# Kernel tuning notes

Measured on AMD Instinct MI355X. Metric: run time of the kernel, lower is better.

Reference implementation:

```python
import jax, jax.numpy as jnp
import numpy as np
import math

B, C_IN, N_SEL, N_DROP, HEADS = 4, 128, 1024, 1024, 4
Q_OUT = K_OUT = V_OUT = 256
N = N_SEL + N_DROP


def setup_inputs() -> dict:
    key = jax.random.key(0)
    ks = jax.random.split(key, 8)
    pcd_up = jax.random.normal(ks[0], (B, C_IN, N), jnp.float32)
    points_select = jax.random.normal(ks[1], (B, C_IN, N_SEL), jnp.float32)
    points_drop = jax.random.normal(ks[2], (B, C_IN, N_DROP), jnp.float32)
    # per-batch permutation of [0, N) split into select/drop halves (collision-free scatter)
    perms = jax.vmap(lambda k: jax.random.permutation(k, N))(jax.random.split(ks[3], B))
    idx_select = perms[:, None, :N_SEL].astype(jnp.int32)
    idx_drop = perms[:, None, N_SEL:].astype(jnp.int32)
    scale = 1.0 / math.sqrt(C_IN)
    Wq = jax.random.normal(ks[4], (Q_OUT, C_IN), jnp.float32) * scale
    Wk = jax.random.normal(ks[5], (K_OUT, C_IN), jnp.float32) * scale
    Wv = jax.random.normal(ks[6], (V_OUT, C_IN), jnp.float32) * scale
    Wskip = jax.random.normal(ks[7], (V_OUT, C_IN), jnp.float32) * scale
    return {"pcd_up": pcd_up, "points_select": points_select, "points_drop": points_drop,
            "idx_select": idx_select, "idx_drop": idx_drop,
            "Wq": Wq, "Wk": Wk, "Wv": Wv, "Wskip": Wskip}


def _concat_by_idx(a, b, idx_a, idx_b):
    # scatter columns of concat([a,b]) to positions given by concat([idx_a, idx_b])
    src = jnp.concatenate([a, b], axis=-1)            # (B, C, N)
    idx = jnp.concatenate([idx_a, idx_b], axis=-1)[:, 0, :]  # (B, N)
    return jax.vmap(lambda s, i: jnp.zeros_like(s).at[:, i].set(s))(src, idx)


def reference(pcd_up, points_select, points_drop, idx_select, idx_drop, Wq, Wk, Wv, Wskip):
    b, _, n = pcd_up.shape
    x = _concat_by_idx(points_select, points_drop, idx_select, idx_drop)  # (B, C_in, N)
    # 1x1 convs (no bias) == channel matmuls, then split heads: (B, H, D, N)
    q = jnp.einsum('oc,bcn->bon', Wq, x).reshape(b, HEADS, Q_OUT // HEADS, n)
    k = jnp.einsum('oc,bcn->bon', Wk, x).reshape(b, HEADS, K_OUT // HEADS, n)
    v = jnp.einsum('oc,bcn->bon', Wv, x).reshape(b, HEADS, V_OUT // HEADS, n)
    energy = jnp.einsum('bhdn,bhdm->bhnm', q, k)      # (B, H, N, N)
    attn = jax.nn.softmax(energy / math.sqrt(Q_OUT // HEADS), axis=-1)
    out = jnp.einsum('bhnm,bhdm->bhnd', attn, v)      # (B, H, N, Dv)
    out = out.transpose(0, 2, 1, 3).reshape(b, n, V_OUT).transpose(0, 2, 1)  # (B, V_out, N)
    skip = jnp.einsum('oc,bcn->bon', Wskip, pcd_up)   # (B, V_out, N)
    return skip + out
```

## Files before the change

### kernel.cpp

```cpp
#include <hip/hip_runtime.h>
#include <hip/hip_bf16.h>
#include <math.h>

#define B_    4
#define C_IN_ 128
#define N_    2048
#define NSEL_ 1024
#define H_    4
#define KS_   2

typedef __bf16 bf16;
typedef __bf16 bf16x2 __attribute__((ext_vector_type(2)));
typedef __bf16 bf16x4 __attribute__((ext_vector_type(4)));
typedef __bf16 bf16x8 __attribute__((ext_vector_type(8)));
typedef float  f32x4  __attribute__((ext_vector_type(4)));

__global__ __launch_bounds__(256) void prep_kernel(
    const int* __restrict__ isel, const int* __restrict__ idrp,
    const float* __restrict__ Wq, const float* __restrict__ Wk,
    const float* __restrict__ Wv, const float* __restrict__ Ws,
    int* __restrict__ inv, bf16* __restrict__ Wbf)
{
    const int blk = blockIdx.x;
    if (blk < 128) {
        int e = blk * 256 + threadIdx.x;
        int which = e >> 13, idx = e & 8191;
        const float* Wx = (which == 0) ? Wq : (which == 1) ? Wk
                        : (which == 2) ? Wv : Ws;
        float4 v = *(const float4*)(Wx + (size_t)idx * 4);
        bf16x4 o; o[0] = (bf16)v.x; o[1] = (bf16)v.y; o[2] = (bf16)v.z; o[3] = (bf16)v.w;
        *(bf16x4*)(Wbf + (size_t)which * 32768 + (size_t)idx * 4) = o;
    } else {
        int g = (blk - 128) * 256 + threadIdx.x;
        int b = g >> 11, j = g & (N_ - 1);
        int pos = (j < NSEL_) ? isel[b * NSEL_ + j] : idrp[b * NSEL_ + (j - NSEL_)];
        inv[b * N_ + (pos & (N_ - 1))] = j;
    }
}

#define XSTR 136

__global__ __launch_bounds__(256) void qkv_mfma_kernel(
    const float* __restrict__ pcd, const float* __restrict__ sel,
    const float* __restrict__ drop, const bf16* __restrict__ Wbf,
    bf16* __restrict__ qT, bf16* __restrict__ kTt, bf16* __restrict__ vTt)
{
    const int ntile = blockIdx.x;
    const int which = blockIdx.y >> 1;
    const int rh    = blockIdx.y & 1;
    const int b     = blockIdx.z;
    const int tid   = threadIdx.x;
    const int w     = tid >> 6;
    const int lane  = tid & 63;
    const int quad  = lane >> 4;
    const int lc    = lane & 15;
    const int n0    = ntile * 64;

    __shared__ __align__(16) bf16 xT[64 * XSTR];

    const float* srcp; int rstride;
    if (ntile < 16) { srcp = sel  + (size_t)b * C_IN_ * NSEL_ + n0;           rstride = NSEL_; }
    else            { srcp = drop + (size_t)b * C_IN_ * NSEL_ + (n0 - NSEL_); rstride = NSEL_; }

    #pragma unroll
    for (int k = 0; k < 4; ++k) {
        int e  = tid + k * 256;
        int cp = e >> 4, nq = e & 15;
        int c0 = cp * 2;
        float4 v0 = *(const float4*)(srcp + (size_t)c0 * rstride + nq * 4);
        float4 v1 = *(const float4*)(srcp + (size_t)(c0 + 1) * rstride + nq * 4);
        int cc = c0 ^ ((nq & 3) << 3);
        float a0[4] = {v0.x, v0.y, v0.z, v0.w};
        float a1[4] = {v1.x, v1.y, v1.z, v1.w};
        #pragma unroll
        for (int i = 0; i < 4; ++i) {
            int n = nq * 4 + i;
            bf16x2 t; t[0] = (bf16)a0[i]; t[1] = (bf16)a1[i];
            *(bf16x2*)&xT[n * XSTR + cc] = t;
        }
    }
    __syncthreads();

    const bf16* wbase = Wbf + (size_t)which * 256 * 128;
    const int rbase = rh * 128 + w * 32;

    f32x4 acc[8];
    #pragma unroll
    for (int i = 0; i < 8; ++i) acc[i] = (f32x4){0.f, 0.f, 0.f, 0.f};

    #pragma unroll
    for (int kq = 0; kq < 4; ++kq) {
        bf16x8 wf[2], xA[4];
        #pragma unroll
        for (int ot = 0; ot < 2; ++ot)
            wf[ot] = *(const bf16x8*)(wbase + (size_t)(rbase + ot * 16 + lc) * 128 + kq * 32 + quad * 8);
        #pragma unroll
        for (int nt = 0; nt < 4; ++nt) {
            int row = nt * 16 + lc;
            int col = (kq * 32 + quad * 8) ^ (((row >> 2) & 3) << 3);
            xA[nt] = *(const bf16x8*)&xT[row * XSTR + col];
        }
        if (which <= 1) {
            #pragma unroll
            for (int nt = 0; nt < 4; ++nt)
                #pragma unroll
                for (int ot = 0; ot < 2; ++ot)
                    acc[nt * 2 + ot] = __builtin_amdgcn_mfma_f32_16x16x32_bf16(xA[nt], wf[ot], acc[nt * 2 + ot], 0, 0, 0);
        } else {
            #pragma unroll
            for (int ot = 0; ot < 2; ++ot)
                #pragma unroll
                for (int nt = 0; nt < 4; ++nt)
                    acc[ot * 4 + nt] = __builtin_amdgcn_mfma_f32_16x16x32_bf16(wf[ot], xA[nt], acc[ot * 4 + nt], 0, 0, 0);
        }
    }

    if (which <= 1) {
        #pragma unroll
        for (int nt = 0; nt < 4; ++nt) {
            #pragma unroll
            for (int ot = 0; ot < 2; ++ot) {
                #pragma unroll
                for (int r = 0; r < 4; ++r) {
                    int n    = n0 + nt * 16 + quad * 4 + r;
                    int rloc = nt * 16 + quad * 4 + r;
                    int o256 = rbase + ot * 16 + lc;
                    int h = o256 >> 6, d = o256 & 63;
                    float val = acc[nt * 2 + ot][r];
                    if (which == 0)
                        qT[((size_t)(b * H_ + h) * N_ + n) * 64 + d] = (bf16)(val * 0.125f);
                    else
                        kTt[(((size_t)(b * H_ + h) * 32 + ntile) << 12) | (rloc << 6) | d] = (bf16)val;
                }
            }
        }
    } else {
        #pragma unroll
        for (int ot = 0; ot < 2; ++ot) {
            #pragma unroll
            for (int r = 0; r < 4; ++r) {
                int o256 = rbase + ot * 16 + quad * 4 + r;
                int h = o256 >> 6, dv = o256 & 63;
                bf16x4 pk;
                #pragma unroll
                for (int nt = 0; nt < 4; ++nt) pk[nt] = (bf16)acc[ot * 4 + nt][r];
                *(bf16x4*)(vTt + ((((size_t)(b * H_ + h) * 32 + ntile) << 12) | (dv << 6) | (lc * 4))) = pk;
            }
        }
    }
}

#define PSTR 72
#define KVSTR 72

__global__ __launch_bounds__(256, 2) void attn_kernel(
    const bf16* __restrict__ qT, const bf16* __restrict__ kTt,
    const bf16* __restrict__ vTt, bf16* __restrict__ Opart,
    float* __restrict__ S_ws)
{
    const int id    = blockIdx.x;
    const int bh    = (id & 7) + 8 * ((id >> 3) & 1);
    const int qb    = (id >> 4) & 15;
    const int c     = id >> 8;
    const int b     = bh >> 2;
    const int h     = bh & 3;
    const int tid   = threadIdx.x;
    const int w     = tid >> 6;
    const int lane  = tid & 63;
    const int quad  = lane >> 4;
    const int lc    = lane & 15;
    const int n0    = qb * 128 + w * 32;

    __shared__ __align__(16) bf16 sK[2][64 * KVSTR];
    __shared__ __align__(16) bf16 sV[2][64 * KVSTR];
    __shared__ __align__(16) bf16 p_lds[4 * 16 * PSTR];
    bf16* pw = &p_lds[w * 16 * PSTR];

    bf16x8 aq[2][2];
    #pragma unroll
    for (int t = 0; t < 2; ++t) {
        const bf16* qp = qT + ((size_t)bh * N_ + n0 + t * 16 + lc) * 64 + quad * 8;
        aq[t][0] = *(const bf16x8*)(qp);
        aq[t][1] = *(const bf16x8*)(qp + 32);
    }

    const bf16* kbase = kTt + (((size_t)bh * 32 + c * 16) << 12);
    const bf16* vbase = vTt + (((size_t)bh * 32 + c * 16) << 12);

    const int l0 = (tid >> 3) * KVSTR + (tid & 7) * 8;
    const int l1 = ((tid >> 3) + 32) * KVSTR + (tid & 7) * 8;

    bf16x8 ldK0 = *(const bf16x8*)(kbase + tid * 8);
    bf16x8 ldK1 = *(const bf16x8*)(kbase + 2048 + tid * 8);
    bf16x8 ldV0 = *(const bf16x8*)(vbase + tid * 8);
    bf16x8 ldV1 = *(const bf16x8*)(vbase + 2048 + tid * 8);

    f32x4 accO[2][4];
    #pragma unroll
    for (int t = 0; t < 2; ++t)
        #pragma unroll
        for (int i = 0; i < 4; ++i) accO[t][i] = (f32x4){0.f, 0.f, 0.f, 0.f};
    float psum[2][4] = {{0.f,0.f,0.f,0.f},{0.f,0.f,0.f,0.f}};

    for (int s = 0; s < 16; ++s) {
        const int buf = s & 1;
        *(bf16x8*)&sK[buf][l0] = ldK0;
        *(bf16x8*)&sK[buf][l1] = ldK1;
        *(bf16x8*)&sV[buf][l0] = ldV0;
        *(bf16x8*)&sV[buf][l1] = ldV1;
        __syncthreads();

        if (s < 15) {
            const bf16* kg = kbase + ((size_t)(s + 1) << 12);
            const bf16* vg = vbase + ((size_t)(s + 1) << 12);
            ldK0 = *(const bf16x8*)(kg + tid * 8);
            ldK1 = *(const bf16x8*)(kg + 2048 + tid * 8);
            ldV0 = *(const bf16x8*)(vg + tid * 8);
            ldV1 = *(const bf16x8*)(vg + 2048 + tid * 8);
        }

        bf16x8 kf[4][2], vf[4][2];
        #pragma unroll
        for (int mt = 0; mt < 4; ++mt) {
            const int rb = (mt * 16 + lc) * KVSTR + quad * 8;
            kf[mt][0] = *(const bf16x8*)&sK[buf][rb];
            kf[mt][1] = *(const bf16x8*)&sK[buf][rb + 32];
            vf[mt][0] = *(const bf16x8*)&sV[buf][rb];
            vf[mt][1] = *(const bf16x8*)&sV[buf][rb + 32];
        }

        #pragma unroll
        for (int t = 0; t < 2; ++t) {
            f32x4 accS[4];
            #pragma unroll
            for (int mt = 0; mt < 4; ++mt) {
                f32x4 z = (f32x4){0.f, 0.f, 0.f, 0.f};
                z = __builtin_amdgcn_mfma_f32_16x16x32_bf16(aq[t][0], kf[mt][0], z, 0, 0, 0);
                z = __builtin_amdgcn_mfma_f32_16x16x32_bf16(aq[t][1], kf[mt][1], z, 0, 0, 0);
                accS[mt] = z;
            }
            #pragma unroll
            for (int r = 0; r < 4; ++r) {
                float sum = 0.f;
                #pragma unroll
                for (int mt = 0; mt < 4; ++mt) {
                    float p = __expf(accS[mt][r]);
                    accS[mt][r] = p;
                    sum += p;
                }
                psum[t][r] += sum;
            }
            #pragma unroll
            for (int r = 0; r < 4; ++r) {
                bf16x4 pk;
                #pragma unroll
                for (int mt = 0; mt < 4; ++mt) pk[mt] = (bf16)accS[mt][r];
                *(bf16x4*)&pw[(quad * 4 + r) * PSTR + lc * 4] = pk;
            }
            bf16x8 ap0 = *(const bf16x8*)(&pw[lc * PSTR + quad * 8]);
            bf16x8 ap1 = *(const bf16x8*)(&pw[lc * PSTR + 32 + quad * 8]);
            #pragma unroll
            for (int dvt = 0; dvt < 4; ++dvt) {
                accO[t][dvt] = __builtin_amdgcn_mfma_f32_16x16x32_bf16(ap0, vf[dvt][0], accO[t][dvt], 0, 0, 0);
                accO[t][dvt] = __builtin_amdgcn_mfma_f32_16x16x32_bf16(ap1, vf[dvt][1], accO[t][dvt], 0, 0, 0);
            }
        }
    }

    #pragma unroll
    for (int t = 0; t < 2; ++t) {
        float inv[4];
        #pragma unroll
        for (int r = 0; r < 4; ++r) {
            float s = psum[t][r];
            #pragma unroll
            for (int off = 1; off < 16; off <<= 1)
                s += __shfl_xor(s, off, 64);
            inv[r] = 1.f / s;
            int n = n0 + t * 16 + quad * 4 + r;
            if (lc == 0)
                S_ws[((size_t)(c * B_ + b) * H_ + h) * N_ + n] = s;
        }
        #pragma unroll
        for (int r = 0; r < 4; ++r) {
            int n = n0 + t * 16 + quad * 4 + r;
            #pragma unroll
            for (int dvt = 0; dvt < 4; ++dvt) {
                int o = h * 64 + dvt * 16 + lc;
                Opart[((size_t)(c * B_ + b) * N_ + n) * 256 + o] = (bf16)(accO[t][dvt][r] * inv[r]);
            }
        }
    }
}

__global__ __launch_bounds__(256) void scatter_kernel(
    const bf16* __restrict__ Opart, const float* __restrict__ S_ws,
    const int* __restrict__ inv, const float* __restrict__ pcd,
    const bf16* __restrict__ Wbf, float* __restrict__ out)
{
    const int ptile = blockIdx.x;
    const int og    = blockIdx.y;
    const int b     = blockIdx.z;
    const int tid   = threadIdx.x;
    const int w     = tid >> 6;
    const int lane  = tid & 63;
    const int quad  = lane >> 4;
    const int lc    = lane & 15;
    const int p0    = ptile * 64;

    __shared__ __align__(16) bf16 xT[64 * XSTR];
    __shared__ __align__(16) bf16 lds[64 * 72];
    __shared__ float wls[KS_][64];
    __shared__ int   jrow[64];

    const float* srcp = pcd + (size_t)b * C_IN_ * N_ + p0;
    #pragma unroll
    for (int k = 0; k < 4; ++k) {
        int e  = tid + k * 256;
        int cp = e >> 4, nq = e & 15;
        int c0 = cp * 2;
        float4 v0 = *(const float4*)(srcp + (size_t)c0 * N_ + nq * 4);
        float4 v1 = *(const float4*)(srcp + (size_t)(c0 + 1) * N_ + nq * 4);
        int cc = c0 ^ ((nq & 3) << 3);
        float a0[4] = {v0.x, v0.y, v0.z, v0.w};
        float a1[4] = {v1.x, v1.y, v1.z, v1.w};
        #pragma unroll
        for (int i = 0; i < 4; ++i) {
            int n = nq * 4 + i;
            bf16x2 t; t[0] = (bf16)a0[i]; t[1] = (bf16)a1[i];
            *(bf16x2*)&xT[n * XSTR + cc] = t;
        }
    }
    if (tid < 64) {
        int row = tid;
        int j = inv[b * N_ + p0 + row] & (N_ - 1);
        jrow[row] = j;
        float sv[KS_]; float denom = 0.f;
        #pragma unroll
        for (int c = 0; c < KS_; ++c) {
            sv[c] = S_ws[((size_t)(c * B_ + b) * H_ + og) * N_ + j];
            denom += sv[c];
        }
        float idn = 1.f / denom;
        #pragma unroll
        for (int c = 0; c < KS_; ++c) wls[c][row] = sv[c] * idn;
    }
    __syncthreads();

    const bf16* wbase = Wbf + (size_t)3 * 256 * 128 + (size_t)(og * 64 + w * 16) * 128;
    f32x4 acc[4];
    #pragma unroll
    for (int i = 0; i < 4; ++i) acc[i] = (f32x4){0.f, 0.f, 0.f, 0.f};
    #pragma unroll
    for (int kq = 0; kq < 4; ++kq) {
        bf16x8 A = *(const bf16x8*)(wbase + (size_t)lc * 128 + kq * 32 + quad * 8);
        #pragma unroll
        for (int nt = 0; nt < 4; ++nt) {
            int row = nt * 16 + lc;
            int col = (kq * 32 + quad * 8) ^ (((row >> 2) & 3) << 3);
            bf16x8 Bf = *(const bf16x8*)&xT[row * XSTR + col];
            acc[nt] = __builtin_amdgcn_mfma_f32_16x16x32_bf16(A, Bf, acc[nt], 0, 0, 0);
        }
    }

    #pragma unroll
    for (int k = 0; k < 2; ++k) {
        int e = tid + k * 256;
        int row = e >> 3, seg = e & 7;
        int j = jrow[row];
        float a8[8];
        #pragma unroll
        for (int i = 0; i < 8; ++i) a8[i] = 0.f;
        #pragma unroll
        for (int c = 0; c < KS_; ++c) {
            bf16x8 v = *(const bf16x8*)(Opart + ((size_t)(c * B_ + b) * N_ + j) * 256 + og * 64 + seg * 8);
            float wgt = wls[c][row];
            #pragma unroll
            for (int i = 0; i < 8; ++i) a8[i] += wgt * (float)v[i];
        }
        bf16x8 o8;
        #pragma unroll
        for (int i = 0; i < 8; ++i) o8[i] = (bf16)a8[i];
        *(bf16x8*)&lds[row * 72 + seg * 8] = o8;
    }
    __syncthreads();

    #pragma unroll
    for (int nt = 0; nt < 4; ++nt) {
        #pragma unroll
        for (int r = 0; r < 4; ++r) {
            int o_loc = w * 16 + quad * 4 + r;
            int p     = nt * 16 + lc;
            float attn = (float)lds[p * 72 + o_loc];
            out[((size_t)b * 256 + og * 64 + o_loc) * N_ + p0 + p] = acc[nt][r] + attn;
        }
    }
}

extern "C" void kernel_launch(void* const* d_in, const int* in_sizes, int n_in,
                              void* d_out, int out_size, void* d_ws, size_t ws_size,
                              hipStream_t stream) {
    const float* pcd  = (const float*)d_in[0];
    const float* sel  = (const float*)d_in[1];
    const float* drop = (const float*)d_in[2];
    const int*   isel = (const int*)d_in[3];
    const int*   idrp = (const int*)d_in[4];
    const float* Wq   = (const float*)d_in[5];
    const float* Wk   = (const float*)d_in[6];
    const float* Wv   = (const float*)d_in[7];
    const float* Ws   = (const float*)d_in[8];
    float* out = (float*)d_out;

    const size_t MB = 1024 * 1024;
    char*  ws    = (char*)d_ws;
    bf16*  qT    = (bf16*)(ws);
    bf16*  kTt   = (bf16*)(ws + 4 * MB);
    bf16*  vTt   = (bf16*)(ws + 8 * MB);
    bf16*  Opart = (bf16*)(ws + 12 * MB);
    float* S_ws  = (float*)(ws + 20 * MB);
    bf16*  Wbf   = (bf16*)(ws + 20 * MB + 256 * 1024);
    int*   inv   = (int*)(ws + 20 * MB + 512 * 1024);

    prep_kernel<<<dim3(160), 256, 0, stream>>>(isel, idrp, Wq, Wk, Wv, Ws, inv, Wbf);
    qkv_mfma_kernel<<<dim3(32, 6, B_), 256, 0, stream>>>(pcd, sel, drop, Wbf,
                                                         qT, kTt, vTt);
    attn_kernel<<<dim3(16 * 16 * KS_), 256, 0, stream>>>(qT, kTt, vTt, Opart, S_ws);
    scatter_kernel<<<dim3(32, 4, B_), 256, 0, stream>>>(Opart, S_ws, inv, pcd, Wbf, out);
}
```

Measured before the change: 117.9 us.

## Double attention query tile per block and move inverse-index build into QKV kernel

The attention kernel now gives each wave 64 query rows instead of 32, so each staged K/V tile in LDS serves twice as many queries. The grid halves to 256 blocks and launch bounds drop to one block per CU, which allows more registers per thread. Separately, the inverse-permutation scatter moves out of the prep kernel into an extra y-slice of the QKV kernel, taking that work off the prep kernel's path. The risks are lower occupancy and fewer blocks than the CU count, which may leave compute units idle and weaken latency hiding.

```diff
diff --git a/kernel.cpp b/kernel.cpp
--- a/kernel.cpp
+++ b/kernel.cpp
@@ -16,40 +16,44 @@
 typedef float  f32x4  __attribute__((ext_vector_type(4)));
 
 __global__ __launch_bounds__(256) void prep_kernel(
-    const int* __restrict__ isel, const int* __restrict__ idrp,
     const float* __restrict__ Wq, const float* __restrict__ Wk,
     const float* __restrict__ Wv, const float* __restrict__ Ws,
-    int* __restrict__ inv, bf16* __restrict__ Wbf)
+    bf16* __restrict__ Wbf)
 {
-    const int blk = blockIdx.x;
-    if (blk < 128) {
-        int e = blk * 256 + threadIdx.x;
-        int which = e >> 13, idx = e & 8191;
-        const float* Wx = (which == 0) ? Wq : (which == 1) ? Wk
-                        : (which == 2) ? Wv : Ws;
-        float4 v = *(const float4*)(Wx + (size_t)idx * 4);
-        bf16x4 o; o[0] = (bf16)v.x; o[1] = (bf16)v.y; o[2] = (bf16)v.z; o[3] = (bf16)v.w;
-        *(bf16x4*)(Wbf + (size_t)which * 32768 + (size_t)idx * 4) = o;
-    } else {
-        int g = (blk - 128) * 256 + threadIdx.x;
-        int b = g >> 11, j = g & (N_ - 1);
-        int pos = (j < NSEL_) ? isel[b * NSEL_ + j] : idrp[b * NSEL_ + (j - NSEL_)];
-        inv[b * N_ + (pos & (N_ - 1))] = j;
-    }
+    int e = blockIdx.x * 256 + threadIdx.x;
+    int which = e >> 13, idx = e & 8191;
+    const float* Wx = (which == 0) ? Wq : (which == 1) ? Wk
+                    : (which == 2) ? Wv : Ws;
+    float4 v = *(const float4*)(Wx + (size_t)idx * 4);
+    bf16x4 o; o[0] = (bf16)v.x; o[1] = (bf16)v.y; o[2] = (bf16)v.z; o[3] = (bf16)v.w;
+    *(bf16x4*)(Wbf + (size_t)which * 32768 + (size_t)idx * 4) = o;
 }
 
 #define XSTR 136
 
 __global__ __launch_bounds__(256) void qkv_mfma_kernel(
-    const float* __restrict__ pcd, const float* __restrict__ sel,
-    const float* __restrict__ drop, const bf16* __restrict__ Wbf,
-    bf16* __restrict__ qT, bf16* __restrict__ kTt, bf16* __restrict__ vTt)
+    const float* __restrict__ sel, const float* __restrict__ drop,
+    const bf16* __restrict__ Wbf,
+    const int* __restrict__ isel, const int* __restrict__ idrp,
+    bf16* __restrict__ qT, bf16* __restrict__ kTt, bf16* __restrict__ vTt,
+    int* __restrict__ inv)
 {
     const int ntile = blockIdx.x;
+    const int b     = blockIdx.z;
+    const int tid   = threadIdx.x;
+
+    if (blockIdx.y == 6) {
+        if (ntile < 8) {
+            int j = ntile * 256 + tid;
+            int pos = (j < NSEL_) ? isel[b * NSEL_ + j]
+                                  : idrp[b * NSEL_ + (j - NSEL_)];
+            inv[b * N_ + (pos & (N_ - 1))] = j;
+        }
+        return;
+    }
+
     const int which = blockIdx.y >> 1;
     const int rh    = blockIdx.y & 1;
-    const int b     = blockIdx.z;
-    const int tid   = threadIdx.x;
     const int w     = tid >> 6;
     const int lane  = tid & 63;
     const int quad  = lane >> 4;
@@ -153,15 +157,15 @@
 #define PSTR 72
 #define KVSTR 72
 
-__global__ __launch_bounds__(256, 2) void attn_kernel(
+__global__ __launch_bounds__(256, 1) void attn_kernel(
     const bf16* __restrict__ qT, const bf16* __restrict__ kTt,
     const bf16* __restrict__ vTt, bf16* __restrict__ Opart,
     float* __restrict__ S_ws)
 {
     const int id    = blockIdx.x;
     const int bh    = (id & 7) + 8 * ((id >> 3) & 1);
-    const int qb    = (id >> 4) & 15;
-    const int c     = id >> 8;
+    const int qb    = (id >> 4) & 7;
+    const int c     = id >> 7;
     const int b     = bh >> 2;
     const int h     = bh & 3;
     const int tid   = threadIdx.x;
@@ -169,16 +173,16 @@
     const int lane  = tid & 63;
     const int quad  = lane >> 4;
     const int lc    = lane & 15;
-    const int n0    = qb * 128 + w * 32;
+    const int n0    = qb * 256 + w * 64;
 
     __shared__ __align__(16) bf16 sK[2][64 * KVSTR];
     __shared__ __align__(16) bf16 sV[2][64 * KVSTR];
     __shared__ __align__(16) bf16 p_lds[4 * 16 * PSTR];
     bf16* pw = &p_lds[w * 16 * PSTR];
 
-    bf16x8 aq[2][2];
-    #pragma unroll
-    for (int t = 0; t < 2; ++t) {
+    bf16x8 aq[4][2];
+    #pragma unroll
+    for (int t = 0; t < 4; ++t) {
         const bf16* qp = qT + ((size_t)bh * N_ + n0 + t * 16 + lc) * 64 + quad * 8;
         aq[t][0] = *(const bf16x8*)(qp);
         aq[t][1] = *(const bf16x8*)(qp + 32);
@@ -195,12 +199,16 @@
     bf16x8 ldV0 = *(const bf16x8*)(vbase + tid * 8);
     bf16x8 ldV1 = *(const bf16x8*)(vbase + 2048 + tid * 8);
 
-    f32x4 accO[2][4];
-    #pragma unroll
-    for (int t = 0; t < 2; ++t)
+    f32x4 accO[4][4];
+    #pragma unroll
+    for (int t = 0; t < 4; ++t)
         #pragma unroll
         for (int i = 0; i < 4; ++i) accO[t][i] = (f32x4){0.f, 0.f, 0.f, 0.f};
-    float psum[2][4] = {{0.f,0.f,0.f,0.f},{0.f,0.f,0.f,0.f}};
+    float psum[4][4];
+    #pragma unroll
+    for (int t = 0; t < 4; ++t)
+        #pragma unroll
+        for (int r = 0; r < 4; ++r) psum[t][r] = 0.f;
 
     for (int s = 0; s < 16; ++s) {
         const int buf = s & 1;
@@ -230,7 +238,7 @@
         }
 
         #pragma unroll
-        for (int t = 0; t < 2; ++t) {
+        for (int t = 0; t < 4; ++t) {
             f32x4 accS[4];
             #pragma unroll
             for (int mt = 0; mt < 4; ++mt) {
@@ -268,15 +276,15 @@
     }
 
     #pragma unroll
-    for (int t = 0; t < 2; ++t) {
-        float inv[4];
+    for (int t = 0; t < 4; ++t) {
+        float inv4[4];
         #pragma unroll
         for (int r = 0; r < 4; ++r) {
             float s = psum[t][r];
             #pragma unroll
             for (int off = 1; off < 16; off <<= 1)
                 s += __shfl_xor(s, off, 64);
-            inv[r] = 1.f / s;
+            inv4[r] = 1.f / s;
             int n = n0 + t * 16 + quad * 4 + r;
             if (lc == 0)
                 S_ws[((size_t)(c * B_ + b) * H_ + h) * N_ + n] = s;
@@ -287,7 +295,7 @@
             #pragma unroll
             for (int dvt = 0; dvt < 4; ++dvt) {
                 int o = h * 64 + dvt * 16 + lc;
-                Opart[((size_t)(c * B_ + b) * N_ + n) * 256 + o] = (bf16)(accO[t][dvt][r] * inv[r]);
+                Opart[((size_t)(c * B_ + b) * N_ + n) * 256 + o] = (bf16)(accO[t][dvt][r] * inv4[r]);
             }
         }
     }
@@ -421,9 +429,10 @@
     bf16*  Wbf   = (bf16*)(ws + 20 * MB + 256 * 1024);
     int*   inv   = (int*)(ws + 20 * MB + 512 * 1024);
 
-    prep_kernel<<<dim3(160), 256, 0, stream>>>(isel, idrp, Wq, Wk, Wv, Ws, inv, Wbf);
-    qkv_mfma_kernel<<<dim3(32, 6, B_), 256, 0, stream>>>(pcd, sel, drop, Wbf,
-                                                         qT, kTt, vTt);
-    attn_kernel<<<dim3(16 * 16 * KS_), 256, 0, stream>>>(qT, kTt, vTt, Opart, S_ws);
+    prep_kernel<<<dim3(128), 256, 0, stream>>>(Wq, Wk, Wv, Ws, Wbf);
+    qkv_mfma_kernel<<<dim3(32, 7, B_), 256, 0, stream>>>(sel, drop, Wbf,
+                                                         isel, idrp,
+                                                         qT, kTt, vTt, inv);
+    attn_kernel<<<dim3(16 * 8 * KS_), 256, 0, stream>>>(qT, kTt, vTt, Opart, S_ws);
     scatter_kernel<<<dim3(32, 4, B_), 256, 0, stream>>>(Opart, S_ws, inv, pcd, Wbf, out);
 }
```

Result: slower. 125.7 us (+6.6%).
